# Optimization experiments

Measured on AMD Instinct MI355X. Metric: run time of the kernel, lower is better.

## Reference

```python
import jax, jax.numpy as jnp
import numpy as np

KS = 3          # kernel_size
PAD = KS // 2   # =1, symmetric pad (pd=2, pdr=1 in the original)


def setup_inputs() -> dict:
    key = jax.random.key(0)
    k1, k2 = jax.random.split(key)
    B, H, W, T, C = 1, 48, 48, 48, 32
    q = jax.random.normal(k1, (B, H, W, T, C), dtype=jnp.float32)
    k = jax.random.normal(k2, (B, H, W, T, C), dtype=jnp.float32)
    return {"q": q, "k": k}


def reference(q, k):
    # q, k: [B, H, W, T, C]
    B, H, W, T, C = q.shape
    # zero-pad k spatially by 1 on each side (matches nnf.pad with pdr=1)
    kp = jnp.pad(k, ((0, 0), (PAD, PAD), (PAD, PAD), (PAD, PAD), (0, 0)))
    # gather the 27 shifted windows; token order (dh major, dt minor) matches
    # unfold(1).unfold(2).unfold(3) + permute in the original.
    wins = jnp.stack(
        [kp[:, a:a + H, b:b + W, c:c + T, :]
         for a in range(KS) for b in range(KS) for c in range(KS)],
        axis=4,
    )  # [B, H, W, T, 27, C]
    # QK^T over channel dim -> [B, H, W, T, 27]
    scores = jnp.einsum('bhwtc,bhwtjc->bhwtj', q, wins)
    attn = jax.nn.softmax(scores, axis=-1)
    # fixed displacement grid v: offsets (-1,0,1)^3 in (dh, dw, dt) order
    ax = jnp.arange(-(KS // 2), KS // 2 + 1, dtype=q.dtype)  # [-1, 0, 1]
    offs = jnp.stack(jnp.meshgrid(ax, ax, ax, indexing='ij'), axis=-1)
    offs = offs.reshape(KS ** 3, 3)  # [27, 3]
    # displacement-weighted sum -> [B, H, W, T, 3]
    x = jnp.einsum('bhwtj,jd->bhwtd', attn, offs)
    # -> [B, 3, H, W, T]
    return jnp.transpose(x, (0, 4, 1, 2, 3))
```

## Files before the change

kernel.cpp:

```cpp
#include <hip/hip_runtime.h>
#include <hip/hip_bf16.h>
#include <math.h>

#define DH 48
#define DW 48
#define DT 48
#define DC 32
#define NPOS (DH * DW * DT)

__global__ __launch_bounds__(384) void cotr_natt_kernel(
    const float* __restrict__ q,
    const float* __restrict__ k,
    float* __restrict__ out)
{
    const int h = blockIdx.x / DW;
    const int w = blockIdx.x - h * DW;
    const int t = threadIdx.x >> 3;
    const int sub = threadIdx.x & 7;

    const int idx = (h * DW + w) * DT + t;

    const float4 qv =
        *reinterpret_cast<const float4*>(q + (size_t)idx * DC + sub * 4);

    float part[27];
#pragma unroll
    for (int a = 0; a < 3; ++a) {
        const int hh = h + a - 1;
        const bool va = ((unsigned)hh < DH);
#pragma unroll
        for (int b = 0; b < 3; ++b) {
            const int ww = w + b - 1;
            const bool vab = va && ((unsigned)ww < DW);
            const float* krow = k + (size_t)(hh * DW + ww) * DT * DC;
#pragma unroll
            for (int c = 0; c < 3; ++c) {
                const int tt = t + c - 1;
                const int j = (a * 3 + b) * 3 + c;
                float s = 0.0f;
                if (vab & ((unsigned)tt < DT)) {
                    const float4 kv = *reinterpret_cast<const float4*>(
                        krow + (size_t)tt * DC + sub * 4);
                    s = fmaf(qv.x, kv.x,
                        fmaf(qv.y, kv.y,
                        fmaf(qv.z, kv.z, qv.w * kv.w)));
                }
                part[j] = s;
            }
        }
    }

    float m = -INFINITY;
#pragma unroll
    for (int j = 0; j < 27; ++j) {
        float v = part[j];
        v += __shfl_xor(v, 1, 64);
        v += __shfl_xor(v, 2, 64);
        v += __shfl_xor(v, 4, 64);
        part[j] = v;
        m = fmaxf(m, v);
    }

    float sum = 0.0f;
    float oh = 0.0f, ow = 0.0f, ot = 0.0f;
#pragma unroll
    for (int j = 0; j < 27; ++j) {
        const float e = __expf(part[j] - m);
        sum += e;
        const float da = (float)(j / 9 - 1);
        const float db = (float)((j / 3) % 3 - 1);
        const float dc = (float)(j % 3 - 1);
        oh = fmaf(e, da, oh);
        ow = fmaf(e, db, ow);
        ot = fmaf(e, dc, ot);
    }
    const float inv = 1.0f / sum;

    if (sub == 0)      out[0 * NPOS + idx] = oh * inv;
    else if (sub == 1) out[1 * NPOS + idx] = ow * inv;
    else if (sub == 2) out[2 * NPOS + idx] = ot * inv;
}

extern "C" void kernel_launch(void* const* d_in, const int* in_sizes, int n_in,
                              void* d_out, int out_size, void* d_ws, size_t ws_size,
                              hipStream_t stream) {
    const float* q = reinterpret_cast<const float*>(d_in[0]);
    const float* k = reinterpret_cast<const float*>(d_in[1]);
    float* out = reinterpret_cast<float*>(d_out);

    const int threads = 384;
    const int blocks = DH * DW;
    cotr_natt_kernel<<<blocks, threads, 0, stream>>>(q, k, out);
}
```

Before: 94.49 us.

## Stage 3D k halo tiles in shared memory for neighborhood attention

Each block now covers a 2x4x4 tile of output positions and loads its 4x6x6 k halo into LDS once, with clamped indices. All 27 neighbor dot products then read from shared memory instead of global memory. Out-of-bounds neighbors are handled by multiplying their scores by a 0/1 mask, which matches zero padding because a zero k vector gives a zero score. This trades many repeated global loads served by L1/L2 for one cooperative halo load plus a barrier, and the halo is 4.5x larger than the tile.

```diff
diff --git a/kernel.cpp b/kernel.cpp
--- a/kernel.cpp
+++ b/kernel.cpp
@@ -8,46 +8,88 @@
 #define DC 32
 #define NPOS (DH * DW * DT)
 
-__global__ __launch_bounds__(384) void cotr_natt_kernel(
+#define TH 2
+#define TW 4
+#define TT 4
+#define LH (TH + 2)
+#define LW (TW + 2)
+#define LT (TT + 2)
+#define NLINES (LH * LW * LT)
+#define NF4 (NLINES * 8)
+#define NTHREADS (TH * TW * TT * 8)
+
+__global__ __launch_bounds__(NTHREADS) void cotr_natt_kernel(
     const float* __restrict__ q,
     const float* __restrict__ k,
     float* __restrict__ out)
 {
-    const int h = blockIdx.x / DW;
-    const int w = blockIdx.x - h * DW;
-    const int t = threadIdx.x >> 3;
-    const int sub = threadIdx.x & 7;
+    __shared__ float kl[NLINES * DC];
 
+    const int bt = blockIdx.x % (DT / TT);
+    const int bw = (blockIdx.x / (DT / TT)) % (DW / TW);
+    const int bh = blockIdx.x / ((DT / TT) * (DW / TW));
+    const int h0 = bh * TH, w0 = bw * TW, t0 = bt * TT;
+
+    const int tid = threadIdx.x;
+    const int p = tid >> 3;
+    const int sub = tid & 7;
+    const int lh = p >> 4;
+    const int lw = (p >> 2) & 3;
+    const int lt = p & 3;
+    const int h = h0 + lh, w = w0 + lw, t = t0 + lt;
     const int idx = (h * DW + w) * DT + t;
 
     const float4 qv =
         *reinterpret_cast<const float4*>(q + (size_t)idx * DC + sub * 4);
 
+    float4 tmp[5];
+#pragma unroll
+    for (int i = 0; i < 5; ++i) {
+        const int s = i * NTHREADS + tid;
+        if (s < NF4) {
+            const int line = s >> 3, c4 = s & 7;
+            const int llt = line % LT;
+            const int llw = (line / LT) % LW;
+            const int llh = line / (LT * LW);
+            const int hh = min(max(h0 + llh - 1, 0), DH - 1);
+            const int ww = min(max(w0 + llw - 1, 0), DW - 1);
+            const int tt = min(max(t0 + llt - 1, 0), DT - 1);
+            tmp[i] = *reinterpret_cast<const float4*>(
+                k + ((size_t)(hh * DW + ww) * DT + tt) * DC + c4 * 4);
+        }
+    }
+#pragma unroll
+    for (int i = 0; i < 5; ++i) {
+        const int s = i * NTHREADS + tid;
+        if (s < NF4)
+            *reinterpret_cast<float4*>(&kl[s * 4]) = tmp[i];
+    }
+    __syncthreads();
+
     float part[27];
 #pragma unroll
     for (int a = 0; a < 3; ++a) {
-        const int hh = h + a - 1;
-        const bool va = ((unsigned)hh < DH);
 #pragma unroll
         for (int b = 0; b < 3; ++b) {
-            const int ww = w + b - 1;
-            const bool vab = va && ((unsigned)ww < DW);
-            const float* krow = k + (size_t)(hh * DW + ww) * DT * DC;
 #pragma unroll
             for (int c = 0; c < 3; ++c) {
-                const int tt = t + c - 1;
-                const int j = (a * 3 + b) * 3 + c;
-                float s = 0.0f;
-                if (vab & ((unsigned)tt < DT)) {
-                    const float4 kv = *reinterpret_cast<const float4*>(
-                        krow + (size_t)tt * DC + sub * 4);
-                    s = fmaf(qv.x, kv.x,
-                        fmaf(qv.y, kv.y,
-                        fmaf(qv.z, kv.z, qv.w * kv.w)));
-                }
-                part[j] = s;
+                const int line = ((lh + a) * LW + (lw + b)) * LT + (lt + c);
+                const float4 kv = *reinterpret_cast<const float4*>(
+                    &kl[line * DC + sub * 4]);
+                part[(a * 3 + b) * 3 + c] =
+                    fmaf(qv.x, kv.x,
+                    fmaf(qv.y, kv.y,
+                    fmaf(qv.z, kv.z, qv.w * kv.w)));
             }
         }
+    }
+
+    float as_[3], bs_[3], cs_[3];
+#pragma unroll
+    for (int u = 0; u < 3; ++u) {
+        as_[u] = ((unsigned)(h + u - 1) < DH) ? 1.0f : 0.0f;
+        bs_[u] = ((unsigned)(w + u - 1) < DW) ? 1.0f : 0.0f;
+        cs_[u] = ((unsigned)(t + u - 1) < DT) ? 1.0f : 0.0f;
     }
 
     float m = -INFINITY;
@@ -57,6 +99,7 @@
         v += __shfl_xor(v, 1, 64);
         v += __shfl_xor(v, 2, 64);
         v += __shfl_xor(v, 4, 64);
+        v *= as_[j / 9] * bs_[(j / 3) % 3] * cs_[j % 3];
         part[j] = v;
         m = fmaxf(m, v);
     }
@@ -88,7 +131,6 @@
     const float* k = reinterpret_cast<const float*>(d_in[1]);
     float* out = reinterpret_cast<float*>(d_out);
 
-    const int threads = 384;
-    const int blocks = DH * DW;
-    cotr_natt_kernel<<<blocks, threads, 0, stream>>>(q, k, out);
+    const int blocks = (DH / TH) * (DW / TW) * (DT / TT);
+    cotr_natt_kernel<<<blocks, NTHREADS, 0, stream>>>(q, k, out);
 }
```

New measurement: 105.9 us. +12.0%, slower.

## Tile 3D blocks, compute two T-adjacent queries per thread, drop softmax max pass

Applied to the files above, without the earlier changes.

Each block now covers an 8x8x4 spatial tile, and each pair of threads splits the 32 channels. Every thread computes two neighboring t positions, so the overlapping key rows are loaded once and reused for both queries. The cross-lane reduction moves from three shuffles to a single DPP quad-permute add, and the dot products use packed two-wide FMAs. Softmax now accumulates exp directly, with no separate max pass or per-score storage. That removes registers and a full loop but loses overflow protection if scores become very large.

```diff
diff --git a/kernel.cpp b/kernel.cpp
--- a/kernel.cpp
+++ b/kernel.cpp
@@ -8,77 +8,127 @@
 #define DC 32
 #define NPOS (DH * DW * DT)
 
-__global__ __launch_bounds__(384) void cotr_natt_kernel(
+typedef float f32x2 __attribute__((ext_vector_type(2)));
+
+template <int CTRL>
+__device__ __forceinline__ float qperm_add(float v) {
+    const int s = __builtin_amdgcn_update_dpp(
+        0, __float_as_int(v), CTRL, 0xF, 0xF, true);
+    return v + __int_as_float(s);
+}
+
+__device__ __forceinline__ float dot16(const float4 a0, const float4 a1,
+                                       const float4 a2, const float4 a3,
+                                       const float4 b0, const float4 b1,
+                                       const float4 b2, const float4 b3) {
+    f32x2 acc = {0.f, 0.f};
+    acc = __builtin_elementwise_fma((f32x2){a0.x, a0.y}, (f32x2){b0.x, b0.y}, acc);
+    acc = __builtin_elementwise_fma((f32x2){a0.z, a0.w}, (f32x2){b0.z, b0.w}, acc);
+    acc = __builtin_elementwise_fma((f32x2){a1.x, a1.y}, (f32x2){b1.x, b1.y}, acc);
+    acc = __builtin_elementwise_fma((f32x2){a1.z, a1.w}, (f32x2){b1.z, b1.w}, acc);
+    acc = __builtin_elementwise_fma((f32x2){a2.x, a2.y}, (f32x2){b2.x, b2.y}, acc);
+    acc = __builtin_elementwise_fma((f32x2){a2.z, a2.w}, (f32x2){b2.z, b2.w}, acc);
+    acc = __builtin_elementwise_fma((f32x2){a3.x, a3.y}, (f32x2){b3.x, b3.y}, acc);
+    acc = __builtin_elementwise_fma((f32x2){a3.z, a3.w}, (f32x2){b3.z, b3.w}, acc);
+    return acc.x + acc.y;
+}
+
+__global__ __launch_bounds__(256, 4) void cotr_natt_kernel(
     const float* __restrict__ q,
     const float* __restrict__ k,
     float* __restrict__ out)
 {
-    const int h = blockIdx.x / DW;
-    const int w = blockIdx.x - h * DW;
-    const int t = threadIdx.x >> 3;
-    const int sub = threadIdx.x & 7;
+    const int tid = threadIdx.x;
+    const int sub = tid & 1;
+    const int col = tid >> 1;
+    const int ct  = col & 1;
+    const int cw  = (col >> 1) & 7;
+    const int ch2 = col >> 4;
 
-    const int idx = (h * DW + w) * DT + t;
+    const int bt = blockIdx.x % (DT / 4);
+    const int bw = (blockIdx.x / (DT / 4)) % (DW / 8);
+    const int bh = blockIdx.x / ((DT / 4) * (DW / 8));
 
-    const float4 qv =
-        *reinterpret_cast<const float4*>(q + (size_t)idx * DC + sub * 4);
+    const int h = bh * 8 + ch2;
+    const int w = bw * 8 + cw;
+    const int tb = bt * 4 + ct * 2;
 
-    float part[27];
+    const int idx0 = (h * DW + w) * DT + tb;
+
+    const float4* qp0 =
+        reinterpret_cast<const float4*>(q + (size_t)idx0 * DC) + sub * 4;
+    const float4 qA0 = qp0[0], qA1 = qp0[1], qA2 = qp0[2], qA3 = qp0[3];
+    const float4 qB0 = qp0[8], qB1 = qp0[9], qB2 = qp0[10], qB3 = qp0[11];
+
+    int ttc[4];
+    float tv[4];
+#pragma unroll
+    for (int l = 0; l < 4; ++l) {
+        const int tt = tb - 1 + l;
+        ttc[l] = min(max(tt, 0), DT - 1);
+        tv[l] = ((unsigned)tt < DT) ? 1.0f : 0.0f;
+    }
+
+    float s0 = 0.f, oh0 = 0.f, ow0 = 0.f, ot0 = 0.f;
+    float s1 = 0.f, oh1 = 0.f, ow1 = 0.f, ot1 = 0.f;
+
 #pragma unroll
     for (int a = 0; a < 3; ++a) {
         const int hh = h + a - 1;
-        const bool va = ((unsigned)hh < DH);
+        const float fa = ((unsigned)hh < DH) ? 1.0f : 0.0f;
+        const int hc = min(max(hh, 0), DH - 1);
 #pragma unroll
         for (int b = 0; b < 3; ++b) {
             const int ww = w + b - 1;
-            const bool vab = va && ((unsigned)ww < DW);
-            const float* krow = k + (size_t)(hh * DW + ww) * DT * DC;
+            const float fab = fa * (((unsigned)ww < DW) ? 1.0f : 0.0f);
+            const int wc = min(max(ww, 0), DW - 1);
+            const int rb = (hc * DW + wc) * DT;
 #pragma unroll
-            for (int c = 0; c < 3; ++c) {
-                const int tt = t + c - 1;
-                const int j = (a * 3 + b) * 3 + c;
-                float s = 0.0f;
-                if (vab & ((unsigned)tt < DT)) {
-                    const float4 kv = *reinterpret_cast<const float4*>(
-                        krow + (size_t)tt * DC + sub * 4);
-                    s = fmaf(qv.x, kv.x,
-                        fmaf(qv.y, kv.y,
-                        fmaf(qv.z, kv.z, qv.w * kv.w)));
+            for (int l = 0; l < 4; ++l) {
+                const float4* kp = reinterpret_cast<const float4*>(
+                    k + (size_t)(rb + ttc[l]) * DC) + sub * 4;
+                const float4 k0 = kp[0], k1 = kp[1], k2 = kp[2], k3 = kp[3];
+                const float sc = fab * tv[l];
+                if (l <= 2) {
+                    float d = dot16(qA0, qA1, qA2, qA3, k0, k1, k2, k3);
+                    d = qperm_add<0xB1>(d);
+                    const float e = __expf(d * sc);
+                    s0 += e;
+                    if (a == 0) oh0 -= e;
+                    if (a == 2) oh0 += e;
+                    if (b == 0) ow0 -= e;
+                    if (b == 2) ow0 += e;
+                    if (l == 0) ot0 -= e;
+                    if (l == 2) ot0 += e;
                 }
-                part[j] = s;
+                if (l >= 1) {
+                    float d = dot16(qB0, qB1, qB2, qB3, k0, k1, k2, k3);
+                    d = qperm_add<0xB1>(d);
+                    const float e = __expf(d * sc);
+                    s1 += e;
+                    if (a == 0) oh1 -= e;
+                    if (a == 2) oh1 += e;
+                    if (b == 0) ow1 -= e;
+                    if (b == 2) ow1 += e;
+                    if (l == 1) ot1 -= e;
+                    if (l == 3) ot1 += e;
+                }
             }
         }
     }
 
-    float m = -INFINITY;
-#pragma unroll
-    for (int j = 0; j < 27; ++j) {
-        float v = part[j];
-        v += __shfl_xor(v, 1, 64);
-        v += __shfl_xor(v, 2, 64);
-        v += __shfl_xor(v, 4, 64);
-        part[j] = v;
-        m = fmaxf(m, v);
+    const float i0 = 1.0f / s0;
+    const float i1 = 1.0f / s1;
+
+    if (sub == 0) {
+        out[0 * NPOS + idx0]     = oh0 * i0;
+        out[0 * NPOS + idx0 + 1] = oh1 * i1;
+        out[1 * NPOS + idx0]     = ow0 * i0;
+        out[1 * NPOS + idx0 + 1] = ow1 * i1;
+    } else {
+        out[2 * NPOS + idx0]     = ot0 * i0;
+        out[2 * NPOS + idx0 + 1] = ot1 * i1;
     }
-
-    float sum = 0.0f;
-    float oh = 0.0f, ow = 0.0f, ot = 0.0f;
-#pragma unroll
-    for (int j = 0; j < 27; ++j) {
-        const float e = __expf(part[j] - m);
-        sum += e;
-        const float da = (float)(j / 9 - 1);
-        const float db = (float)((j / 3) % 3 - 1);
-        const float dc = (float)(j % 3 - 1);
-        oh = fmaf(e, da, oh);
-        ow = fmaf(e, db, ow);
-        ot = fmaf(e, dc, ot);
-    }
-    const float inv = 1.0f / sum;
-
-    if (sub == 0)      out[0 * NPOS + idx] = oh * inv;
-    else if (sub == 1) out[1 * NPOS + idx] = ow * inv;
-    else if (sub == 2) out[2 * NPOS + idx] = ot * inv;
 }
 
 extern "C" void kernel_launch(void* const* d_in, const int* in_sizes, int n_in,
@@ -88,7 +138,6 @@
     const float* k = reinterpret_cast<const float*>(d_in[1]);
     float* out = reinterpret_cast<float*>(d_out);
 
-    const int threads = 384;
-    const int blocks = DH * DW;
-    cotr_natt_kernel<<<blocks, threads, 0, stream>>>(q, k, out);
+    const int blocks = (DH / 8) * (DW / 8) * (DT / 4);
+    cotr_natt_kernel<<<blocks, 256, 0, stream>>>(q, k, out);
 }
```

After: 87.51 us. 1.08x faster.
